# Kernel tuning notes

Measured on AMD Instinct MI355X. Metric: run time of the kernel, lower is better.

## Reference

```python
import jax, jax.numpy as jnp
import numpy as np

HEADS, HEAD_DIM, NQP, NVP = 12, 16, 4, 8
NODE_DIM, EDGE_DIM = 384, 128
B, N = 1, 768


def setup_inputs() -> dict:
    key = jax.random.key(0)
    ks = jax.random.split(key, 12)
    node_features = jax.random.normal(ks[0], (B, N, NODE_DIM), dtype=jnp.float32)
    edge_features = jax.random.normal(ks[1], (B, N, N, EDGE_DIM), dtype=jnp.float32)
    # random valid rotations via QR of gaussian matrices (well-conditioned for inverse)
    A = jax.random.normal(ks[2], (B, N, 3, 3), dtype=jnp.float32)
    Q, _ = jnp.linalg.qr(A)
    R = Q
    t = jax.random.normal(ks[3], (B, N, 3), dtype=jnp.float32)
    def lin(k, din, dout):
        return jax.random.normal(k, (din, dout), dtype=jnp.float32) / np.sqrt(din)
    Wqkv = lin(ks[4], NODE_DIM, 3 * HEADS * HEAD_DIM)
    Wvqk = lin(ks[5], NODE_DIM, 2 * 3 * NQP * HEADS)
    Wvv = lin(ks[6], NODE_DIM, 3 * NVP * HEADS)
    Webias = lin(ks[7], EDGE_DIM, HEADS)
    fin_in = HEADS * EDGE_DIM + HEADS * HEAD_DIM + HEADS * NVP * 4
    Wfin = lin(ks[8], fin_in, NODE_DIM)
    bfin = jnp.zeros((NODE_DIM,), dtype=jnp.float32)
    return {"node_features": node_features, "edge_features": edge_features,
            "R": R, "t": t, "Wqkv": Wqkv, "Wvqk": Wvqk, "Wvv": Wvv,
            "Webias": Webias, "Wfin": Wfin, "bfin": bfin}


def _ipa(node_features, edge_features, R, t, Wqkv, Wvqk, Wvv, Webias, Wfin, bfin):
    b, n, _ = node_features.shape
    h, d, p, pv = HEADS, HEAD_DIM, NQP, NVP
    # scalar q, k, v: [b, h, n, d]
    qkv = (node_features @ Wqkv).reshape(b, n, 3, h, d)
    sq, sk, sv = [jnp.transpose(qkv[:, :, i], (0, 2, 1, 3)) for i in range(3)]
    node_scalar = jnp.einsum('bhid,bhjd->bhij', sq, sk) * (d ** -0.5)
    edge_bias = jnp.einsum('bijd,dh->bhij', edge_features, Webias)
    # vector q/k in local frames: [b, h, n, p, 3]
    vqk = (node_features @ Wvqk).reshape(b, n, 2, h, p, 3)
    vq = jnp.transpose(vqk[:, :, 0], (0, 2, 1, 3, 4))
    vk = jnp.transpose(vqk[:, :, 1], (0, 2, 1, 3, 4))
    t_e = t[:, None, :, None, :]  # [b,1,n,1,3]
    gq = jnp.einsum('bnij,bhnpj->bhnpi', R, vq) + t_e
    gk = jnp.einsum('bnij,bhnpj->bhnpi', R, vk) + t_e
    # ||gk_i - gq_j||^2 summed over (p,3), expanded to avoid [b,h,n,n,p,3]
    wc = np.sqrt(2.0 / 9.0 / p) / 2.0
    k_sq = jnp.sum(gk * gk, axis=(-1, -2))  # [b,h,n]
    q_sq = jnp.sum(gq * gq, axis=(-1, -2))  # [b,h,n]
    cross = jnp.einsum('bhipd,bhjpd->bhij', gk, gq)
    dist = (k_sq[:, :, :, None] + q_sq[:, :, None, :] - 2.0 * cross) * wc
    attn = jax.nn.softmax((node_scalar + edge_bias - dist) * (3 ** -0.5), axis=-1)
    # aggregations
    edge_out = jnp.einsum('bhij,bijd->bihd', attn, edge_features)     # [b,n,h,edge_dim]
    scalar_out = jnp.einsum('bhij,bhjd->bihd', attn, sv)              # [b,n,h,d]
    vv = (node_features @ Wvv).reshape(b, n, h, pv, 3)
    vv = jnp.transpose(vv, (0, 2, 1, 3, 4))                            # [b,h,n,pv,3]
    gvv = jnp.einsum('bnij,bhnpj->bhnpi', R, vv) + t_e
    att_v = jnp.einsum('bhij,bhjpd->bihpd', attn, gvv)                # [b,n,h,pv,3]
    Rinv = jnp.linalg.inv(R)
    local_v = jnp.einsum('bnij,bnhpj->bnhpi', Rinv, att_v - t[:, :, None, None, :])
    v_len = jnp.sqrt(jnp.sum(local_v * local_v, axis=-1))             # [b,n,h,pv]
    combined = jnp.concatenate([
        edge_out.reshape(b, n, -1),
        scalar_out.reshape(b, n, -1),
        local_v.reshape(b, n, -1),
        v_len.reshape(b, n, -1),
    ], axis=-1)
    return node_features + combined @ Wfin + bfin


def reference(node_features, edge_features, R, t, Wqkv, Wvqk, Wvv, Webias, Wfin, bfin):
    return _ipa(node_features, edge_features, R, t, Wqkv, Wvqk, Wvv, Webias, Wfin, bfin)
```

## Files before the change

### kernel.cpp

```cpp
#include <hip/hip_runtime.h>
#include <cmath>


namespace {

constexpr int NN = 768;
constexpr int NH = 12;

constexpr float S3 = 0.5773502691896258f;
constexpr float C1 = 0.25f * S3;
constexpr float C2 = 0.23570226039551584f * S3;
constexpr float C3 = 0.11785113019775792f * S3;

typedef float f32x4 __attribute__((ext_vector_type(4)));
typedef short bf16x8 __attribute__((ext_vector_type(8)));
typedef unsigned int u32x4 __attribute__((ext_vector_type(4)));
typedef unsigned int u32x2 __attribute__((ext_vector_type(2)));
typedef _Float16 f16x2 __attribute__((ext_vector_type(2)));

#define LGKM0 asm volatile("s_waitcnt lgkmcnt(0)" ::: "memory")
#define SCHED0 __builtin_amdgcn_sched_barrier(0)

__device__ inline unsigned cvt_pk_bf16(float lo, float hi) {
  unsigned r;
  asm volatile("v_cvt_pk_bf16_f32 %0, %1, %2" : "=v"(r) : "v"(lo), "v"(hi));
  return r;
}

__device__ inline float fdot2(unsigned a, unsigned b, float c) {
#if __has_builtin(__builtin_amdgcn_fdot2)
  return __builtin_amdgcn_fdot2(__builtin_bit_cast(f16x2, a),
                                __builtin_bit_cast(f16x2, b), c, false);
#else
  union U { unsigned u; _Float16 h[2]; } x, y;
  x.u = a; y.u = b;
  return c + (float)x.h[0] * (float)y.h[0] + (float)x.h[1] * (float)y.h[1];
#endif
}

__device__ inline u32x2 tr_read(unsigned addr) {
  u32x2 d;
  asm volatile("ds_read_b64_tr_b16 %0, %1" : "=v"(d) : "v"(addr));
  return d;
}

__device__ inline f32x4 mfma16(u32x2 a, u32x2 b, f32x4 c) {
  asm volatile("v_mfma_f32_16x16x16_bf16 %0, %1, %2, %0"
               : "+v"(c) : "v"(a), "v"(b));
  return c;
}

__device__ inline unsigned pkf16(float a, float b) {
  union U { _Float16 h[2]; unsigned u; } x;
  x.h[0] = (_Float16)a; x.h[1] = (_Float16)b;
  return x.u;
}

__global__ __launch_bounds__(288) void k_proj(const float* __restrict__ node,
    const float* __restrict__ Wqkv, const float* __restrict__ Wvqk,
    const float* __restrict__ Wvv, float* __restrict__ proj) {
  __shared__ __align__(16) float nl[2][384];
  const int i0 = blockIdx.x * 2;
  const int tid = threadIdx.x;
  for (int idx = tid; idx < 2 * 384; idx += 288)
    ((float*)nl)[idx] = node[(size_t)i0 * 384 + idx];
  __syncthreads();
  const int c0 = tid * 4;
  const float* W; int ld, col;
  if (c0 < 576)      { W = Wqkv; ld = 576; col = c0; }
  else if (c0 < 864) { W = Wvqk; ld = 288; col = c0 - 576; }
  else               { W = Wvv;  ld = 288; col = c0 - 864; }
  float4 acc[2];
#pragma unroll
  for (int r = 0; r < 2; ++r) acc[r] = make_float4(0.f, 0.f, 0.f, 0.f);
#pragma unroll 4
  for (int k = 0; k < 384; ++k) {
    const float4 w4 = *(const float4*)&W[(size_t)k * ld + col];
#pragma unroll
    for (int r = 0; r < 2; ++r) {
      const float nv = nl[r][k];
      acc[r].x += nv * w4.x; acc[r].y += nv * w4.y;
      acc[r].z += nv * w4.z; acc[r].w += nv * w4.w;
    }
  }
#pragma unroll
  for (int r = 0; r < 2; ++r)
    *(float4*)&proj[(size_t)(i0 + r) * 1152 + c0] = acc[r];
}

__global__ __launch_bounds__(256) void k_geom(const float* __restrict__ proj,
    const float* __restrict__ R, const float* __restrict__ t,
    const float* __restrict__ Webias,
    unsigned* __restrict__ Bph, unsigned* __restrict__ Sgh,
    float* __restrict__ V, unsigned* __restrict__ WbP) {
  const int gid = blockIdx.x * 256 + threadIdx.x;
  if (blockIdx.x == 0) {
    const int tid = threadIdx.x;
    const int lane = tid & 63, kk = tid >> 6;
    const int colB = lane & 15, gB = lane >> 4;
    u32x4 wv;
#pragma unroll
    for (int e = 0; e < 4; ++e) {
      const int d = kk * 32 + gB * 8 + 2 * e;
      const float lo = (colB < 12) ? S3 * Webias[d * 12 + colB] : 0.f;
      const float hi = (colB < 12) ? S3 * Webias[(d + 1) * 12 + colB] : 0.f;
      wv[e] = cvt_pk_bf16(lo, hi);
    }
    *(u32x4*)&WbP[(size_t)tid * 4] = wv;
  }
  if (gid >= NN * NH) return;
  const int n = gid / NH, h = gid % NH;
  const float* pr = proj + (size_t)n * 1152;
  const float* Rn = R + n * 9;
  const float t0 = t[n * 3 + 0], t1 = t[n * 3 + 1], t2 = t[n * 3 + 2];
  const size_t hn = (size_t)h * NN + n;
  unsigned* bp = Bph + ((size_t)n * NH + h) * 16;
  unsigned* sg = Sgh + ((size_t)n * NH + h) * 16;
#pragma unroll
  for (int m = 0; m < 8; ++m) {
    bp[m] = pkf16(C1 * pr[(12 + h) * 16 + 2 * m], C1 * pr[(12 + h) * 16 + 2 * m + 1]);
    sg[m] = pkf16(pr[h * 16 + 2 * m], pr[h * 16 + 2 * m + 1]);
    V[hn * 40 + 2 * m]     = pr[(24 + h) * 16 + 2 * m];
    V[hn * 40 + 2 * m + 1] = pr[(24 + h) * 16 + 2 * m + 1];
  }
  float gq[12], gk[12];
  float qs = 0.f, ks = 0.f;
#pragma unroll
  for (int p = 0; p < 4; ++p) {
    {
      const float vx = pr[576 + (h * 4 + p) * 3 + 0];
      const float vy = pr[576 + (h * 4 + p) * 3 + 1];
      const float vz = pr[576 + (h * 4 + p) * 3 + 2];
      const float g0 = Rn[0] * vx + Rn[1] * vy + Rn[2] * vz + t0;
      const float g1 = Rn[3] * vx + Rn[4] * vy + Rn[5] * vz + t1;
      const float g2 = Rn[6] * vx + Rn[7] * vy + Rn[8] * vz + t2;
      gq[p * 3 + 0] = g0; gq[p * 3 + 1] = g1; gq[p * 3 + 2] = g2;
      qs += g0 * g0 + g1 * g1 + g2 * g2;
    }
    {
      const float vx = pr[576 + ((12 + h) * 4 + p) * 3 + 0];
      const float vy = pr[576 + ((12 + h) * 4 + p) * 3 + 1];
      const float vz = pr[576 + ((12 + h) * 4 + p) * 3 + 2];
      const float g0 = Rn[0] * vx + Rn[1] * vy + Rn[2] * vz + t0;
      const float g1 = Rn[3] * vx + Rn[4] * vy + Rn[5] * vz + t1;
      const float g2 = Rn[6] * vx + Rn[7] * vy + Rn[8] * vz + t2;
      gk[p * 3 + 0] = g0; gk[p * 3 + 1] = g1; gk[p * 3 + 2] = g2;
      ks += g0 * g0 + g1 * g1 + g2 * g2;
    }
  }
#pragma unroll
  for (int m = 0; m < 6; ++m) {
    bp[8 + m] = pkf16(C2 * gq[2 * m], C2 * gq[2 * m + 1]);
    sg[8 + m] = pkf16(gk[2 * m], gk[2 * m + 1]);
  }
  bp[14] = pkf16(-C3 * qs, 1.0f);
  sg[14] = pkf16(1.0f, -C3 * ks);
  bp[15] = 0u; sg[15] = 0u;
#pragma unroll
  for (int p = 0; p < 8; ++p) {
    const float vx = pr[864 + (h * 8 + p) * 3 + 0];
    const float vy = pr[864 + (h * 8 + p) * 3 + 1];
    const float vz = pr[864 + (h * 8 + p) * 3 + 2];
    V[hn * 40 + 16 + p * 3 + 0] = Rn[0] * vx + Rn[1] * vy + Rn[2] * vz + t0;
    V[hn * 40 + 16 + p * 3 + 1] = Rn[3] * vx + Rn[4] * vy + Rn[5] * vz + t1;
    V[hn * 40 + 16 + p * 3 + 2] = Rn[6] * vx + Rn[7] * vy + Rn[8] * vz + t2;
  }
}

__global__ __launch_bounds__(256, 3) void k_fused(
    const float* __restrict__ edge, const unsigned* __restrict__ WbP,
    const unsigned* __restrict__ Bph, const unsigned* __restrict__ Sgh,
    unsigned* __restrict__ pTu, float* __restrict__ m_t,
    float* __restrict__ eout, float* __restrict__ msm,
    float* __restrict__ linv) {
  __shared__ __align__(16) unsigned char wreg[4][4224];
  const int i = blockIdx.x;
  const int tid = threadIdx.x;
  const int lane = tid & 63;
  const int w = __builtin_amdgcn_readfirstlane(tid >> 6);
  const int g = lane >> 4;
  const int c16 = lane & 15;
  const int hc = c16 < 12 ? c16 : 11;

  unsigned short* etSw = (unsigned short*)&wreg[w][0];
  const unsigned etbase =
      (unsigned)(uintptr_t)(__attribute__((address_space(3))) unsigned char*)&wreg[w][0];

  bf16x8 wbfrag[4];
#pragma unroll
  for (int kk = 0; kk < 4; ++kk)
    wbfrag[kk] = __builtin_bit_cast(bf16x8,
        *(const u32x4*)&WbP[(size_t)(kk * 64 + lane) * 4]);

  const unsigned* sgp = Sgh + ((size_t)i * NH + hc) * 16;
  const u32x4 sg0 = *(const u32x4*)(sgp + 0);
  const u32x4 sg1 = *(const u32x4*)(sgp + 4);
  const u32x4 sg2 = *(const u32x4*)(sgp + 8);
  const u32x4 sg3 = *(const u32x4*)(sgp + 12);

  float m = -3.0e38f;
  float lsum = 0.f;
  f32x4 acc[8];
#pragma unroll
  for (int dt = 0; dt < 8; ++dt) acc[dt] = (f32x4){0.f, 0.f, 0.f, 0.f};

  float4 ra[8];
  auto load8 = [&](int t) {
    const int jw = t * 64 + w * 16;
#pragma unroll
    for (int q = 0; q < 4; ++q) {
      const int f8 = lane + 64 * q;
      const int j = f8 >> 4, c8 = f8 & 15;
      const float* gp = &edge[((size_t)(i * NN + jw + j)) * 128 + c8 * 8];
      ra[2 * q]     = *(const float4*)gp;
      ra[2 * q + 1] = *(const float4*)(gp + 4);
    }
  };
  auto store8 = [&]() {
#pragma unroll
    for (int q = 0; q < 4; ++q) {
      const int f8 = lane + 64 * q;
      const int j = f8 >> 4, c8 = f8 & 15;
      u32x4 pk;
      pk.x = cvt_pk_bf16(ra[2 * q].x,     ra[2 * q].y);
      pk.y = cvt_pk_bf16(ra[2 * q].z,     ra[2 * q].w);
      pk.z = cvt_pk_bf16(ra[2 * q + 1].x, ra[2 * q + 1].y);
      pk.w = cvt_pk_bf16(ra[2 * q + 1].z, ra[2 * q + 1].w);
      *(u32x4*)&etSw[(c8 >> 1) * 264 + j * 16 + 8 * (c8 & 1)] = pk;
    }
  };

  load8(0);

#pragma unroll 1
  for (int t = 0; t < 12; ++t) {
    const int tw = t * 4 + w;
    LGKM0;
    store8();
    SCHED0;
    if (t < 11) load8(t + 1);

    f32x4 ebacc = {0.f, 0.f, 0.f, 0.f};
#pragma unroll
    for (int kk = 0; kk < 4; ++kk) {
      const int dt = 2 * kk + (g >> 1);
      const bf16x8 a = *(const bf16x8*)&etSw[dt * 264 + c16 * 16 + 8 * (g & 1)];
      ebacc = __builtin_amdgcn_mfma_f32_16x16x32_bf16(a, wbfrag[kk], ebacc, 0, 0, 0);
    }

    float lg[4];
#pragma unroll
    for (int r = 0; r < 4; ++r) {
      const unsigned* bpp = Bph + ((size_t)(tw * 16 + 4 * g + r) * NH + hc) * 16;
      const u32x4 b0 = *(const u32x4*)(bpp + 0);
      const u32x4 b1 = *(const u32x4*)(bpp + 4);
      const u32x4 b2 = *(const u32x4*)(bpp + 8);
      const u32x4 b3 = *(const u32x4*)(bpp + 12);
      float a = fdot2(b0.x, sg0.x, 0.f);
      a = fdot2(b0.y, sg0.y, a);
      a = fdot2(b0.z, sg0.z, a); a = fdot2(b0.w, sg0.w, a);
      a = fdot2(b1.x, sg1.x, a); a = fdot2(b1.y, sg1.y, a);
      a = fdot2(b1.z, sg1.z, a); a = fdot2(b1.w, sg1.w, a);
      a = fdot2(b2.x, sg2.x, a); a = fdot2(b2.y, sg2.y, a);
      a = fdot2(b2.z, sg2.z, a); a = fdot2(b2.w, sg2.w, a);
      a = fdot2(b3.x, sg3.x, a); a = fdot2(b3.y, sg3.y, a);
      a = fdot2(b3.z, sg3.z, a);
      lg[r] = a + ebacc[r];
    }

    const float lmax = fmaxf(fmaxf(lg[0], lg[1]), fmaxf(lg[2], lg[3]));
    if (__any(lmax > m + 6.f)) {
      float tm = lmax;
      tm = fmaxf(tm, __shfl_xor(tm, 16, 64));
      tm = fmaxf(tm, __shfl_xor(tm, 32, 64));
      const float mn = fmaxf(m, tm);
      const float f = __expf(m - mn);
      m = mn;
      lsum *= f;
      float fr[4];
#pragma unroll
      for (int r = 0; r < 4; ++r) fr[r] = __shfl(f, 4 * g + r, 64);
#pragma unroll
      for (int dt = 0; dt < 8; ++dt) {
        acc[dt][0] *= fr[0]; acc[dt][1] *= fr[1];
        acc[dt][2] *= fr[2]; acc[dt][3] *= fr[3];
      }
    }
    float p0 = __expf(lg[0] - m), p1 = __expf(lg[1] - m);
    float p2 = __expf(lg[2] - m), p3 = __expf(lg[3] - m);
    lsum += (p0 + p1) + (p2 + p3);
    const unsigned pk0 = cvt_pk_bf16(p0, p1);
    const unsigned pk1 = cvt_pk_bf16(p2, p3);
    pTu[((size_t)i * 48 + tw) * 128 + g * 16 + c16]      = pk0;
    pTu[((size_t)i * 48 + tw) * 128 + 64 + g * 16 + c16] = pk1;
    if (g == 0) m_t[((size_t)i * 48 + tw) * 16 + c16] = m;

    u32x2 apk; apk.x = pk0; apk.y = pk1;
    u32x2 bfr[4];
#pragma unroll
    for (int half = 0; half < 2; ++half) {
#pragma unroll
      for (int q = 0; q < 4; ++q)
        bfr[q] = tr_read(etbase + (unsigned)((half * 4 + q) * 528 + g * 128 + c16 * 8));
      LGKM0; SCHED0;
#pragma unroll
      for (int q = 0; q < 4; ++q)
        acc[half * 4 + q] = mfma16(apk, bfr[q], acc[half * 4 + q]);
    }
  }

  {
    unsigned short* OshW = (unsigned short*)&wreg[w][0];
#pragma unroll
    for (int dt = 0; dt < 8; ++dt) {
      u32x2 pkk;
      pkk.x = cvt_pk_bf16(acc[dt][0], acc[dt][1]);
      pkk.y = cvt_pk_bf16(acc[dt][2], acc[dt][3]);
      *(u32x2*)&OshW[dt * 256 + c16 * 16 + g * 4] = pkk;
    }
    float ls = lsum;
    ls += __shfl_xor(ls, 16, 64);
    ls += __shfl_xor(ls, 32, 64);
    if (lane < 16) {
      *(float*)&wreg[w][4096 + lane * 4] = m;
      *(float*)&wreg[w][4160 + lane * 4] = ls;
    }
  }
  __syncthreads();
  for (int idx = tid; idx < 12 * 128; idx += 256) {
    const int h = idx >> 7, d = idx & 127;
    const int dt = d >> 4, dp = d & 15;
    float mv[4], lv[4], Ov[4];
#pragma unroll
    for (int w2 = 0; w2 < 4; ++w2) {
      mv[w2] = *(const float*)&wreg[w2][4096 + h * 4];
      lv[w2] = *(const float*)&wreg[w2][4160 + h * 4];
      const unsigned short us =
          *(const unsigned short*)&wreg[w2][(dt * 256 + dp * 16 + h) * 2];
      Ov[w2] = __uint_as_float(((unsigned)us) << 16);
    }
    const float mb = fmaxf(fmaxf(mv[0], mv[1]), fmaxf(mv[2], mv[3]));
    const float f0 = __expf(mv[0] - mb), f1 = __expf(mv[1] - mb);
    const float f2 = __expf(mv[2] - mb), f3 = __expf(mv[3] - mb);
    const float lb = lv[0] * f0 + lv[1] * f1 + lv[2] * f2 + lv[3] * f3;
    const float O = Ov[0] * f0 + Ov[1] * f1 + Ov[2] * f2 + Ov[3] * f3;
    eout[(size_t)i * 1536 + h * 128 + d] = O / lb;
    if (d == 0) {
      msm[(size_t)h * NN + i] = mb;
      linv[(size_t)h * NN + i] = 1.0f / lb;
    }
  }
}

__global__ __launch_bounds__(320) void k_scav(const unsigned* __restrict__ pTu,
    const float* __restrict__ m_t, const float* __restrict__ msm,
    const float* __restrict__ linv, const float* __restrict__ V,
    float* __restrict__ scav) {
  __shared__ __align__(16) float At[64][20];
  __shared__ __align__(16) float Vt[64][40];
  __shared__ __align__(16) float red[320 * 8];
  const int i0 = blockIdx.x * 16;
  const int h  = blockIdx.y;
  const int tid = threadIdx.x;
  const int js = tid / 80, rem = tid % 80;
  const int rg = rem / 20, cp = rem % 20;
  float2 a0 = {0.f, 0.f}, a1 = {0.f, 0.f}, a2 = {0.f, 0.f}, a3 = {0.f, 0.f};
  for (int jt = 0; jt < 12; ++jt) {
    __syncthreads();
    for (int idx = tid; idx < 1024; idx += 320) {
      const int r = idx >> 6, jj = idx & 63;
      const int i = i0 + r;
      const int tw = jt * 4 + (jj >> 4);
      const int gg = (jj & 15) >> 2, e = jj & 3;
      const unsigned u = pTu[((size_t)i * 48 + tw) * 128 + (e >> 1) * 64 + gg * 16 + h];
      const float p = __uint_as_float((e & 1) ? (u & 0xffff0000u) : (u << 16));
      const float fac = __expf(m_t[((size_t)i * 48 + tw) * 16 + h] - msm[(size_t)h * NN + i])
                      * linv[(size_t)h * NN + i];
      At[jj][r] = p * fac;
    }
    for (int idx = tid; idx < 2560; idx += 320) {
      const int jj = idx / 40, c = idx % 40;
      Vt[jj][c] = V[((size_t)h * NN + jt * 64 + jj) * 40 + c];
    }
    __syncthreads();
#pragma unroll 4
    for (int s = 0; s < 16; ++s) {
      const int jj = js * 16 + s;
      const float4 a4 = *(const float4*)&At[jj][rg * 4];
      const float2 b2 = *(const float2*)&Vt[jj][cp * 2];
      a0.x += a4.x * b2.x; a0.y += a4.x * b2.y;
      a1.x += a4.y * b2.x; a1.y += a4.y * b2.y;
      a2.x += a4.z * b2.x; a2.y += a4.z * b2.y;
      a3.x += a4.w * b2.x; a3.y += a4.w * b2.y;
    }
  }
  __syncthreads();
  *(float4*)&red[tid * 8 + 0] = make_float4(a0.x, a0.y, a1.x, a1.y);
  *(float4*)&red[tid * 8 + 4] = make_float4(a2.x, a2.y, a3.x, a3.y);
  __syncthreads();
  if (tid < 80) {
    const int rg2 = tid / 20, cp2 = tid % 20;
    float4 s0 = make_float4(0.f, 0.f, 0.f, 0.f), s1 = s0;
#pragma unroll
    for (int q = 0; q < 4; ++q) {
      const float4 r0 = *(const float4*)&red[(tid + q * 80) * 8 + 0];
      const float4 r1 = *(const float4*)&red[(tid + q * 80) * 8 + 4];
      s0.x += r0.x; s0.y += r0.y; s0.z += r0.z; s0.w += r0.w;
      s1.x += r1.x; s1.y += r1.y; s1.z += r1.z; s1.w += r1.w;
    }
    const size_t base = (size_t)h * NN + i0 + rg2 * 4;
    *(float2*)&scav[(base + 0) * 40 + cp2 * 2] = make_float2(s0.x, s0.y);
    *(float2*)&scav[(base + 1) * 40 + cp2 * 2] = make_float2(s0.z, s0.w);
    *(float2*)&scav[(base + 2) * 40 + cp2 * 2] = make_float2(s1.x, s1.y);
    *(float2*)&scav[(base + 3) * 40 + cp2 * 2] = make_float2(s1.z, s1.w);
  }
}

__global__ __launch_bounds__(256) void k_comb(
    const float* __restrict__ R, const float* __restrict__ t,
    const float* __restrict__ scav, float* __restrict__ combX) {
  const int i0 = blockIdx.x * 4;
  const int tid = threadIdx.x;
  __shared__ float rinv[4][9];
  __shared__ float tl[4][3];
  if (tid < 4) {
    const int i = i0 + tid;
    const float* Rn = R + i * 9;
    const float r00 = Rn[0], r01 = Rn[1], r02 = Rn[2];
    const float r10 = Rn[3], r11 = Rn[4], r12 = Rn[5];
    const float r20 = Rn[6], r21 = Rn[7], r22 = Rn[8];
    const float det = r00 * (r11 * r22 - r12 * r21)
                    - r01 * (r10 * r22 - r12 * r20)
                    + r02 * (r10 * r21 - r11 * r20);
    const float id = 1.0f / det;
    rinv[tid][0] = (r11 * r22 - r12 * r21) * id;
    rinv[tid][1] = (r02 * r21 - r01 * r22) * id;
    rinv[tid][2] = (r01 * r12 - r02 * r11) * id;
    rinv[tid][3] = (r12 * r20 - r10 * r22) * id;
    rinv[tid][4] = (r00 * r22 - r02 * r20) * id;
    rinv[tid][5] = (r02 * r10 - r00 * r12) * id;
    rinv[tid][6] = (r10 * r21 - r11 * r20) * id;
    rinv[tid][7] = (r01 * r20 - r00 * r21) * id;
    rinv[tid][8] = (r00 * r11 - r01 * r10) * id;
    tl[tid][0] = t[i * 3 + 0]; tl[tid][1] = t[i * 3 + 1]; tl[tid][2] = t[i * 3 + 2];
  }
  __syncthreads();
  for (int idx = tid; idx < 4 * 576; idx += 256) {
    const int r = idx / 576, k2 = idx % 576;
    const int i = i0 + r;
    float val;
    if (k2 < 192) {
      const int h = k2 >> 4, d = k2 & 15;
      val = scav[((size_t)h * NN + i) * 40 + d];
    } else if (k2 < 480) {
      const int s = k2 - 192, h = s / 24, rem = s % 24, p = rem / 3, x = rem % 3;
      const float* av = scav + ((size_t)h * NN + i) * 40 + 16 + p * 3;
      const float a0 = av[0] - tl[r][0], a1 = av[1] - tl[r][1], a2 = av[2] - tl[r][2];
      val = rinv[r][x * 3 + 0] * a0 + rinv[r][x * 3 + 1] * a1 + rinv[r][x * 3 + 2] * a2;
    } else {
      const int s = k2 - 480, h = s >> 3, p = s & 7;
      const float* av = scav + ((size_t)h * NN + i) * 40 + 16 + p * 3;
      const float a0 = av[0] - tl[r][0], a1 = av[1] - tl[r][1], a2 = av[2] - tl[r][2];
      const float l0 = rinv[r][0] * a0 + rinv[r][1] * a1 + rinv[r][2] * a2;
      const float l1 = rinv[r][3] * a0 + rinv[r][4] * a1 + rinv[r][5] * a2;
      const float l2 = rinv[r][6] * a0 + rinv[r][7] * a1 + rinv[r][8] * a2;
      val = sqrtf(l0 * l0 + l1 * l1 + l2 * l2);
    }
    combX[(size_t)i * 576 + k2] = val;
  }
}

__global__ __launch_bounds__(256) void k_finalA(
    const float* __restrict__ eout, const float* __restrict__ combX,
    const float* __restrict__ Wfin, float* __restrict__ partial) {
  __shared__ __align__(16) float cl[64][36];
  __shared__ __align__(16) float wl[32][68];
  const int i0 = blockIdx.x * 64;
  const int c0 = blockIdx.y * 64;
  const int k0 = blockIdx.z * 192;
  const float* src; int stride, koff;
  if (blockIdx.z < 8) { src = eout;  stride = 1536; koff = k0; }
  else                { src = combX; stride = 576;  koff = k0 - 1536; }
  const int tid = threadIdx.x;
  const int cq = tid & 15, rq = tid >> 4;
  float4 acc[4];
#pragma unroll
  for (int r = 0; r < 4; ++r) acc[r] = make_float4(0.f, 0.f, 0.f, 0.f);
  for (int sub = 0; sub < 6; ++sub) {
    const int kc = sub * 32;
    __syncthreads();
#pragma unroll
    for (int half = 0; half < 2; ++half) {
      const int qi = tid + half * 256;
      const int r = qi >> 3, kq = qi & 7;
      *(float4*)&cl[r][kq * 4] =
          *(const float4*)&src[(size_t)(i0 + r) * stride + koff + kc + kq * 4];
      const int kk = qi >> 4, cc = qi & 15;
      *(float4*)&wl[kk][cc * 4] =
          *(const float4*)&Wfin[(size_t)(k0 + kc + kk) * 384 + c0 + cc * 4];
    }
    __syncthreads();
#pragma unroll
    for (int k4 = 0; k4 < 8; ++k4) {
      float4 a[4], wv[4];
#pragma unroll
      for (int r = 0; r < 4; ++r) a[r] = *(const float4*)&cl[rq * 4 + r][k4 * 4];
#pragma unroll
      for (int q = 0; q < 4; ++q) wv[q] = *(const float4*)&wl[k4 * 4 + q][cq * 4];
#pragma unroll
      for (int r = 0; r < 4; ++r) {
        acc[r].x += a[r].x * wv[0].x + a[r].y * wv[1].x + a[r].z * wv[2].x + a[r].w * wv[3].x;
        acc[r].y += a[r].x * wv[0].y + a[r].y * wv[1].y + a[r].z * wv[2].y + a[r].w * wv[3].y;
        acc[r].z += a[r].x * wv[0].z + a[r].y * wv[1].z + a[r].z * wv[2].z + a[r].w * wv[3].z;
        acc[r].w += a[r].x * wv[0].w + a[r].y * wv[1].w + a[r].z * wv[2].w + a[r].w * wv[3].w;
      }
    }
  }
#pragma unroll
  for (int r = 0; r < 4; ++r)
    *(float4*)&partial[((size_t)blockIdx.z * NN + i0 + rq * 4 + r) * 384 + c0 + cq * 4] = acc[r];
}

__global__ __launch_bounds__(256) void k_finalB(const float* __restrict__ node,
    const float* __restrict__ partial, const float* __restrict__ bfin,
    float* __restrict__ out) {
  const int gid = blockIdx.x * 256 + threadIdx.x;
  const int i = gid / 96, cq = gid % 96;
  float4 v = *(const float4*)&node[(size_t)i * 384 + cq * 4];
  const float4 b = *(const float4*)&bfin[cq * 4];
  v.x += b.x; v.y += b.y; v.z += b.z; v.w += b.w;
#pragma unroll
  for (int s = 0; s < 11; ++s) {
    const float4 p = *(const float4*)&partial[((size_t)s * NN + i) * 384 + cq * 4];
    v.x += p.x; v.y += p.y; v.z += p.z; v.w += p.w;
  }
  *(float4*)&out[(size_t)i * 384 + cq * 4] = v;
}

}

extern "C" void kernel_launch(void* const* d_in, const int* in_sizes, int n_in,
                              void* d_out, int out_size, void* d_ws, size_t ws_size,
                              hipStream_t stream) {
  const float* node   = (const float*)d_in[0];
  const float* edge   = (const float*)d_in[1];
  const float* R      = (const float*)d_in[2];
  const float* t      = (const float*)d_in[3];
  const float* Wqkv   = (const float*)d_in[4];
  const float* Wvqk   = (const float*)d_in[5];
  const float* Wvv    = (const float*)d_in[6];
  const float* Webias = (const float*)d_in[7];
  const float* Wfin   = (const float*)d_in[8];
  const float* bfin   = (const float*)d_in[9];
  float* out = (float*)d_out;

  float* ws = (float*)d_ws;
  float*    proj = ws;
  float*    V    = proj + 884736;
  unsigned* Bph  = (unsigned*)(V + 368640);
  unsigned* Sgh  = Bph + 147456;
  unsigned* WbP  = Sgh + 147456;
  unsigned* pTu  = WbP + 1024;
  float*    m_t  = (float*)(pTu + 4718592);
  float*    eout = m_t + 589824;
  float*    scav = eout + 1179648;
  float*    msm  = scav + 368640;
  float*    linv = msm + 9216;
  float* combX   = (float*)pTu;
  float* partial = combX + 442368;

  hipLaunchKernelGGL(k_proj, dim3(384), dim3(288), 0, stream,
                     node, Wqkv, Wvqk, Wvv, proj);
  hipLaunchKernelGGL(k_geom, dim3(36), dim3(256), 0, stream,
                     proj, R, t, Webias, Bph, Sgh, V, WbP);
  hipLaunchKernelGGL(k_fused, dim3(768), dim3(256), 0, stream,
                     edge, WbP, Bph, Sgh, pTu, m_t, eout, msm, linv);
  hipLaunchKernelGGL(k_scav, dim3(48, 12), dim3(320), 0, stream,
                     pTu, m_t, msm, linv, V, scav);
  hipLaunchKernelGGL(k_comb, dim3(192), dim3(256), 0, stream,
                     R, t, scav, combX);
  hipLaunchKernelGGL(k_finalA, dim3(12, 6, 11), dim3(256), 0, stream,
                     eout, combX, Wfin, partial);
  hipLaunchKernelGGL(k_finalB, dim3(288), dim3(256), 0, stream,
                     node, partial, bfin, out);
}
```

Measured before the change: 236.4 us.

## Store attention probabilities head-major and fuse frame-combine into scav kernel

The fused attention kernel now writes the bf16 probability tiles and per-tile maxima in a head-major layout that drops the four padded head lanes, so the scav kernel reads contiguous 8-byte chunks per row. The rescale factors are precomputed once per block in shared memory. The separate k_comb kernel is folded into k_scav, which applies the inverse rotation and vector lengths from shared memory and writes combX directly. This removes one launch and the scav intermediate round trip, at the cost of more shared memory and a scattered-column write pattern in the scav epilogue.

```diff
diff --git a/kernel.cpp b/kernel.cpp
--- a/kernel.cpp
+++ b/kernel.cpp
@@ -170,7 +170,7 @@
 __global__ __launch_bounds__(256, 3) void k_fused(
     const float* __restrict__ edge, const unsigned* __restrict__ WbP,
     const unsigned* __restrict__ Bph, const unsigned* __restrict__ Sgh,
-    unsigned* __restrict__ pTu, float* __restrict__ m_t,
+    unsigned* __restrict__ pT2, float* __restrict__ m_t2,
     float* __restrict__ eout, float* __restrict__ msm,
     float* __restrict__ linv) {
   __shared__ __align__(16) unsigned char wreg[4][4224];
@@ -291,9 +291,11 @@
     lsum += (p0 + p1) + (p2 + p3);
     const unsigned pk0 = cvt_pk_bf16(p0, p1);
     const unsigned pk1 = cvt_pk_bf16(p2, p3);
-    pTu[((size_t)i * 48 + tw) * 128 + g * 16 + c16]      = pk0;
-    pTu[((size_t)i * 48 + tw) * 128 + 64 + g * 16 + c16] = pk1;
-    if (g == 0) m_t[((size_t)i * 48 + tw) * 16 + c16] = m;
+    if (c16 < 12) {
+      u32x2 pp; pp.x = pk0; pp.y = pk1;
+      *(u32x2*)&pT2[((size_t)c16 * NN + i) * 384 + tw * 8 + g * 2] = pp;
+      if (g == 0) m_t2[((size_t)c16 * NN + i) * 48 + tw] = m;
+    }
 
     u32x2 apk; apk.x = pk0; apk.y = pk1;
     u32x2 bfr[4];
@@ -352,78 +354,25 @@
   }
 }
 
-__global__ __launch_bounds__(320) void k_scav(const unsigned* __restrict__ pTu,
-    const float* __restrict__ m_t, const float* __restrict__ msm,
+__global__ __launch_bounds__(320) void k_scav(const unsigned* __restrict__ pT2,
+    const float* __restrict__ m_t2, const float* __restrict__ msm,
     const float* __restrict__ linv, const float* __restrict__ V,
-    float* __restrict__ scav) {
+    const float* __restrict__ R, const float* __restrict__ t,
+    float* __restrict__ combX) {
   __shared__ __align__(16) float At[64][20];
   __shared__ __align__(16) float Vt[64][40];
   __shared__ __align__(16) float red[320 * 8];
+  __shared__ __align__(16) float fac[16][48];
+  __shared__ __align__(16) float sc[16][40];
+  __shared__ float rinv[16][9];
+  __shared__ float tl[16][3];
   const int i0 = blockIdx.x * 16;
   const int h  = blockIdx.y;
   const int tid = threadIdx.x;
   const int js = tid / 80, rem = tid % 80;
   const int rg = rem / 20, cp = rem % 20;
-  float2 a0 = {0.f, 0.f}, a1 = {0.f, 0.f}, a2 = {0.f, 0.f}, a3 = {0.f, 0.f};
-  for (int jt = 0; jt < 12; ++jt) {
-    __syncthreads();
-    for (int idx = tid; idx < 1024; idx += 320) {
-      const int r = idx >> 6, jj = idx & 63;
-      const int i = i0 + r;
-      const int tw = jt * 4 + (jj >> 4);
-      const int gg = (jj & 15) >> 2, e = jj & 3;
-      const unsigned u = pTu[((size_t)i * 48 + tw) * 128 + (e >> 1) * 64 + gg * 16 + h];
-      const float p = __uint_as_float((e & 1) ? (u & 0xffff0000u) : (u << 16));
-      const float fac = __expf(m_t[((size_t)i * 48 + tw) * 16 + h] - msm[(size_t)h * NN + i])
-                      * linv[(size_t)h * NN + i];
-      At[jj][r] = p * fac;
-    }
-    for (int idx = tid; idx < 2560; idx += 320) {
-      const int jj = idx / 40, c = idx % 40;
-      Vt[jj][c] = V[((size_t)h * NN + jt * 64 + jj) * 40 + c];
-    }
-    __syncthreads();
-#pragma unroll 4
-    for (int s = 0; s < 16; ++s) {
-      const int jj = js * 16 + s;
-      const float4 a4 = *(const float4*)&At[jj][rg * 4];
-      const float2 b2 = *(const float2*)&Vt[jj][cp * 2];
-      a0.x += a4.x * b2.x; a0.y += a4.x * b2.y;
-      a1.x += a4.y * b2.x; a1.y += a4.y * b2.y;
-      a2.x += a4.z * b2.x; a2.y += a4.z * b2.y;
-      a3.x += a4.w * b2.x; a3.y += a4.w * b2.y;
-    }
-  }
-  __syncthreads();
-  *(float4*)&red[tid * 8 + 0] = make_float4(a0.x, a0.y, a1.x, a1.y);
-  *(float4*)&red[tid * 8 + 4] = make_float4(a2.x, a2.y, a3.x, a3.y);
-  __syncthreads();
-  if (tid < 80) {
-    const int rg2 = tid / 20, cp2 = tid % 20;
-    float4 s0 = make_float4(0.f, 0.f, 0.f, 0.f), s1 = s0;
-#pragma unroll
-    for (int q = 0; q < 4; ++q) {
-      const float4 r0 = *(const float4*)&red[(tid + q * 80) * 8 + 0];
-      const float4 r1 = *(const float4*)&red[(tid + q * 80) * 8 + 4];
-      s0.x += r0.x; s0.y += r0.y; s0.z += r0.z; s0.w += r0.w;
-      s1.x += r1.x; s1.y += r1.y; s1.z += r1.z; s1.w += r1.w;
-    }
-    const size_t base = (size_t)h * NN + i0 + rg2 * 4;
-    *(float2*)&scav[(base + 0) * 40 + cp2 * 2] = make_float2(s0.x, s0.y);
-    *(float2*)&scav[(base + 1) * 40 + cp2 * 2] = make_float2(s0.z, s0.w);
-    *(float2*)&scav[(base + 2) * 40 + cp2 * 2] = make_float2(s1.x, s1.y);
-    *(float2*)&scav[(base + 3) * 40 + cp2 * 2] = make_float2(s1.z, s1.w);
-  }
-}
-
-__global__ __launch_bounds__(256) void k_comb(
-    const float* __restrict__ R, const float* __restrict__ t,
-    const float* __restrict__ scav, float* __restrict__ combX) {
-  const int i0 = blockIdx.x * 4;
-  const int tid = threadIdx.x;
-  __shared__ float rinv[4][9];
-  __shared__ float tl[4][3];
-  if (tid < 4) {
+
+  if (tid < 16) {
     const int i = i0 + tid;
     const float* Rn = R + i * 9;
     const float r00 = Rn[0], r01 = Rn[1], r02 = Rn[2];
@@ -444,29 +393,88 @@
     rinv[tid][8] = (r00 * r11 - r01 * r10) * id;
     tl[tid][0] = t[i * 3 + 0]; tl[tid][1] = t[i * 3 + 1]; tl[tid][2] = t[i * 3 + 2];
   }
+  for (int idx = tid; idx < 768; idx += 320) {
+    const int r = idx / 48, tw = idx % 48;
+    const size_t hi = (size_t)h * NN + i0 + r;
+    fac[r][tw] = __expf(m_t2[hi * 48 + tw] - msm[hi]) * linv[hi];
+  }
+
+  float2 a0 = {0.f, 0.f}, a1 = {0.f, 0.f}, a2 = {0.f, 0.f}, a3 = {0.f, 0.f};
+  for (int jt = 0; jt < 12; ++jt) {
+    __syncthreads();
+    for (int idx = tid; idx < 256; idx += 320) {
+      const int r = idx >> 4, q = idx & 15;
+      const u32x2 v = *(const u32x2*)
+          &pT2[((size_t)h * NN + i0 + r) * 384 + jt * 32 + q * 2];
+      const float fc = fac[r][jt * 4 + (q >> 2)];
+      At[q * 4 + 0][r] = __uint_as_float(v.x << 16) * fc;
+      At[q * 4 + 1][r] = __uint_as_float(v.x & 0xffff0000u) * fc;
+      At[q * 4 + 2][r] = __uint_as_float(v.y << 16) * fc;
+      At[q * 4 + 3][r] = __uint_as_float(v.y & 0xffff0000u) * fc;
+    }
+    for (int idx = tid; idx < 2560; idx += 320) {
+      const int jj = idx / 40, c = idx % 40;
+      Vt[jj][c] = V[((size_t)h * NN + jt * 64 + jj) * 40 + c];
+    }
+    __syncthreads();
+#pragma unroll 4
+    for (int s = 0; s < 16; ++s) {
+      const int jj = js * 16 + s;
+      const float4 a4 = *(const float4*)&At[jj][rg * 4];
+      const float2 b2 = *(const float2*)&Vt[jj][cp * 2];
+      a0.x += a4.x * b2.x; a0.y += a4.x * b2.y;
+      a1.x += a4.y * b2.x; a1.y += a4.y * b2.y;
+      a2.x += a4.z * b2.x; a2.y += a4.z * b2.y;
+      a3.x += a4.w * b2.x; a3.y += a4.w * b2.y;
+    }
+  }
   __syncthreads();
-  for (int idx = tid; idx < 4 * 576; idx += 256) {
-    const int r = idx / 576, k2 = idx % 576;
+  *(float4*)&red[tid * 8 + 0] = make_float4(a0.x, a0.y, a1.x, a1.y);
+  *(float4*)&red[tid * 8 + 4] = make_float4(a2.x, a2.y, a3.x, a3.y);
+  __syncthreads();
+  if (tid < 80) {
+    const int rg2 = tid / 20, cp2 = tid % 20;
+    float4 s0 = make_float4(0.f, 0.f, 0.f, 0.f), s1 = s0;
+#pragma unroll
+    for (int q = 0; q < 4; ++q) {
+      const float4 r0 = *(const float4*)&red[(tid + q * 80) * 8 + 0];
+      const float4 r1 = *(const float4*)&red[(tid + q * 80) * 8 + 4];
+      s0.x += r0.x; s0.y += r0.y; s0.z += r0.z; s0.w += r0.w;
+      s1.x += r1.x; s1.y += r1.y; s1.z += r1.z; s1.w += r1.w;
+    }
+    sc[rg2 * 4 + 0][cp2 * 2] = s0.x; sc[rg2 * 4 + 0][cp2 * 2 + 1] = s0.y;
+    sc[rg2 * 4 + 1][cp2 * 2] = s0.z; sc[rg2 * 4 + 1][cp2 * 2 + 1] = s0.w;
+    sc[rg2 * 4 + 2][cp2 * 2] = s1.x; sc[rg2 * 4 + 2][cp2 * 2 + 1] = s1.y;
+    sc[rg2 * 4 + 3][cp2 * 2] = s1.z; sc[rg2 * 4 + 3][cp2 * 2 + 1] = s1.w;
+  }
+  __syncthreads();
+  for (int idx = tid; idx < 768; idx += 320) {
+    const int r = idx / 48, c = idx % 48;
     const int i = i0 + r;
-    float val;
-    if (k2 < 192) {
-      const int h = k2 >> 4, d = k2 & 15;
-      val = scav[((size_t)h * NN + i) * 40 + d];
-    } else if (k2 < 480) {
-      const int s = k2 - 192, h = s / 24, rem = s % 24, p = rem / 3, x = rem % 3;
-      const float* av = scav + ((size_t)h * NN + i) * 40 + 16 + p * 3;
-      const float a0 = av[0] - tl[r][0], a1 = av[1] - tl[r][1], a2 = av[2] - tl[r][2];
-      val = rinv[r][x * 3 + 0] * a0 + rinv[r][x * 3 + 1] * a1 + rinv[r][x * 3 + 2] * a2;
+    float val; int col;
+    if (c < 16) {
+      val = sc[r][c];
+      col = h * 16 + c;
+    } else if (c < 40) {
+      const int s = c - 16, p = s / 3, x = s % 3;
+      const float a0v = sc[r][16 + p * 3 + 0] - tl[r][0];
+      const float a1v = sc[r][16 + p * 3 + 1] - tl[r][1];
+      const float a2v = sc[r][16 + p * 3 + 2] - tl[r][2];
+      val = rinv[r][x * 3 + 0] * a0v + rinv[r][x * 3 + 1] * a1v
+          + rinv[r][x * 3 + 2] * a2v;
+      col = 192 + h * 24 + s;
     } else {
-      const int s = k2 - 480, h = s >> 3, p = s & 7;
-      const float* av = scav + ((size_t)h * NN + i) * 40 + 16 + p * 3;
-      const float a0 = av[0] - tl[r][0], a1 = av[1] - tl[r][1], a2 = av[2] - tl[r][2];
-      const float l0 = rinv[r][0] * a0 + rinv[r][1] * a1 + rinv[r][2] * a2;
-      const float l1 = rinv[r][3] * a0 + rinv[r][4] * a1 + rinv[r][5] * a2;
-      const float l2 = rinv[r][6] * a0 + rinv[r][7] * a1 + rinv[r][8] * a2;
+      const int p = c - 40;
+      const float a0v = sc[r][16 + p * 3 + 0] - tl[r][0];
+      const float a1v = sc[r][16 + p * 3 + 1] - tl[r][1];
+      const float a2v = sc[r][16 + p * 3 + 2] - tl[r][2];
+      const float l0 = rinv[r][0] * a0v + rinv[r][1] * a1v + rinv[r][2] * a2v;
+      const float l1 = rinv[r][3] * a0v + rinv[r][4] * a1v + rinv[r][5] * a2v;
+      const float l2 = rinv[r][6] * a0v + rinv[r][7] * a1v + rinv[r][8] * a2v;
       val = sqrtf(l0 * l0 + l1 * l1 + l2 * l2);
-    }
-    combX[(size_t)i * 576 + k2] = val;
+      col = 480 + h * 8 + p;
+    }
+    combX[(size_t)i * 576 + col] = val;
   }
 }
 
@@ -560,25 +568,22 @@
   unsigned* Bph  = (unsigned*)(V + 368640);
   unsigned* Sgh  = Bph + 147456;
   unsigned* WbP  = Sgh + 147456;
-  unsigned* pTu  = WbP + 1024;
-  float*    m_t  = (float*)(pTu + 4718592);
-  float*    eout = m_t + 589824;
-  float*    scav = eout + 1179648;
-  float*    msm  = scav + 368640;
+  unsigned* pT2  = WbP + 1024;
+  float*    m_t2 = (float*)(pT2 + 3538944);
+  float*    eout = m_t2 + 442368;
+  float*    msm  = eout + 1179648;
   float*    linv = msm + 9216;
-  float* combX   = (float*)pTu;
-  float* partial = combX + 442368;
+  float*    combX = linv + 9216;
+  float* partial = (float*)pT2;
 
   hipLaunchKernelGGL(k_proj, dim3(384), dim3(288), 0, stream,
                      node, Wqkv, Wvqk, Wvv, proj);
   hipLaunchKernelGGL(k_geom, dim3(36), dim3(256), 0, stream,
                      proj, R, t, Webias, Bph, Sgh, V, WbP);
   hipLaunchKernelGGL(k_fused, dim3(768), dim3(256), 0, stream,
-                     edge, WbP, Bph, Sgh, pTu, m_t, eout, msm, linv);
+                     edge, WbP, Bph, Sgh, pT2, m_t2, eout, msm, linv);
   hipLaunchKernelGGL(k_scav, dim3(48, 12), dim3(320), 0, stream,
-                     pTu, m_t, msm, linv, V, scav);
-  hipLaunchKernelGGL(k_comb, dim3(192), dim3(256), 0, stream,
-                     R, t, scav, combX);
+                     pT2, m_t2, msm, linv, V, R, t, combX);
   hipLaunchKernelGGL(k_finalA, dim3(12, 6, 11), dim3(256), 0, stream,
                      eout, combX, Wfin, partial);
   hipLaunchKernelGGL(k_finalB, dim3(288), dim3(256), 0, stream,
```

Result: faster. 227.4 us (-3.8%).
